# Kernel optimization log

Hardware: AMD Instinct MI355X
Metric: run time of the kernel (lower is better)

Reference implementation:

```python
import jax, jax.numpy as jnp
import numpy as np

T, B, I, H, O = 4096, 16, 64, 256, 1

def setup_inputs() -> dict:
    key = jax.random.key(0)
    ks = jax.random.split(key, 7)
    s_ih = 1.0 / np.sqrt(H)
    return {
        "x": jax.random.normal(ks[0], (T, B, I), dtype=jnp.float32),
        "W_ih": jax.random.normal(ks[1], (4 * H, I), dtype=jnp.float32) * s_ih,
        "W_hh": jax.random.normal(ks[2], (4 * H, H), dtype=jnp.float32) * s_ih,
        "b_ih": jax.random.normal(ks[3], (4 * H,), dtype=jnp.float32) * s_ih,
        "b_hh": jax.random.normal(ks[4], (4 * H,), dtype=jnp.float32) * s_ih,
        "W_lin": jax.random.normal(ks[5], (O, H), dtype=jnp.float32) * s_ih,
        "b_lin": jax.random.normal(ks[6], (O,), dtype=jnp.float32) * s_ih,
        "h0": jnp.zeros((B, H), dtype=jnp.float32),
        "c0": jnp.zeros((B, H), dtype=jnp.float32),
    }

def reference(x, W_ih, W_hh, b_ih, b_hh, W_lin, b_lin, h0, c0):
    # Precompute input contribution for all timesteps: (T, B, 4H)
    x_gates = jnp.einsum('tbi,gi->tbg', x, W_ih) + b_ih + b_hh

    def step(carry, xg):
        h, c = carry
        gates = xg + h @ W_hh.T                      # (B, 4H)
        i, f, g, o = jnp.split(gates, 4, axis=-1)    # PyTorch gate order i|f|g|o
        i = jax.nn.sigmoid(i)
        f = jax.nn.sigmoid(f)
        g = jnp.tanh(g)
        o = jax.nn.sigmoid(o)
        c = f * c + i * g
        h = o * jnp.tanh(c)
        return (h, c), None

    (hT, cT), _ = jax.lax.scan(step, (h0, c0), x_gates)
    # encoder_out[-1] == hT for single-layer unidirectional LSTM; dropout p=0 is identity
    y = jax.nn.sigmoid(hT @ W_lin.T + b_lin)         # (B, O)
    return y
```

## Files before the change

kernel.cpp:

```cpp
#include <hip/hip_runtime.h>
#include <hip/hip_bf16.h>


typedef _Float16 f16x2 __attribute__((ext_vector_type(2)));
typedef _Float16 f16x4 __attribute__((ext_vector_type(4)));
typedef int      i32x4 __attribute__((ext_vector_type(4)));

#define T_STEPS 4096
#define BATCH   16
#define IN      64
#define HID     256
#define G4      1024

__device__ __forceinline__ float fdot2(f16x2 a, f16x2 b, float c) {
#if __has_builtin(__builtin_amdgcn_fdot2)
    return __builtin_amdgcn_fdot2(a, b, c, false);
#else
    return c + (float)a.x * (float)b.x + (float)a.y * (float)b.y;
#endif
}

__device__ __forceinline__ float fast_rcp(float x) {
#if __has_builtin(__builtin_amdgcn_rcpf)
    return __builtin_amdgcn_rcpf(x);
#else
    return 1.0f / x;
#endif
}

__device__ __forceinline__ float sigf(float x) {
    return fast_rcp(1.0f + __expf(-x));
}
__device__ __forceinline__ float tanh_fast(float x) {
    return 2.0f * sigf(2.0f * x) - 1.0f;
}

__global__ __launch_bounds__(256) void xg_precompute(
    const float* __restrict__ x, const float* __restrict__ W_ih,
    const float* __restrict__ b_ih, const float* __restrict__ b_hh,
    _Float16* __restrict__ xg)
{
    const int b   = blockIdx.x;
    const int t0  = blockIdx.y * 128;
    const int tid = threadIdx.x;

    __shared__ __align__(16) f16x2 xs2[IN / 2];

    f16x2 wih[4][32];
    float bias[4];
    const float2* W2 = (const float2*)W_ih;
    #pragma unroll
    for (int g = 0; g < 4; ++g) {
        const int r = tid + g * 256;
        #pragma unroll
        for (int m = 0; m < 32; ++m) {
            float2 v = W2[r * 32 + m];
            wih[g][m] = f16x2{(_Float16)v.x, (_Float16)v.y};
        }
        bias[g] = b_ih[r] + b_hh[r];
    }

    for (int tt = 0; tt < 128; ++tt) {
        const int t = t0 + tt;
        if (tid < 32) {
            float2 v = ((const float2*)x)[(t * BATCH + b) * 32 + tid];
            xs2[tid] = f16x2{(_Float16)v.x, (_Float16)v.y};
        }
        __syncthreads();
        float acc[4] = {bias[0], bias[1], bias[2], bias[3]};
        #pragma unroll
        for (int m = 0; m < 32; ++m) {
            f16x2 xv = xs2[m];
            #pragma unroll
            for (int g = 0; g < 4; ++g) acc[g] = fdot2(wih[g][m], xv, acc[g]);
        }
        f16x4 v4 = f16x4{(_Float16)acc[0], (_Float16)acc[1],
                         (_Float16)acc[2], (_Float16)acc[3]};
        ((f16x4*)xg)[(t * BATCH + b) * 256 + tid] = v4;
        __syncthreads();
    }
}

__global__ __launch_bounds__(1024, 4) void lstm_mfma(
    const float* __restrict__ W_hh,  const float* __restrict__ W_lin,
    const float* __restrict__ b_lin, const float* __restrict__ h0,
    const float* __restrict__ c0,    const _Float16* __restrict__ xg,
    float* __restrict__ out)
{
    const int b   = blockIdx.x;
    const int tid = threadIdx.x;
    const int w   = tid >> 6;
    const int l   = tid & 63;
    const int col = l & 15;
    const int g4  = l >> 4;

    __shared__ __align__(16) signed char hs[2][256];
    __shared__ float esh[256];

    const int u = w * 16 + col;

    const float4* Wh4 = (const float4*)W_hh;
    float qs[4], ksc[4];
    {
        float rm[4];
        #pragma unroll
        for (int g = 0; g < 4; ++g) {
            const int row = g * 256 + u;
            float m = 0.0f;
            #pragma unroll
            for (int c = 0; c < 4; ++c) {
                #pragma unroll
                for (int d = 0; d < 4; ++d) {
                    float4 v = Wh4[row * 64 + 16 * c + 4 * g4 + d];
                    m = fmaxf(m, fmaxf(fmaxf(fabsf(v.x), fabsf(v.y)),
                                       fmaxf(fabsf(v.z), fabsf(v.w))));
                }
            }
            rm[g] = m;
        }
        #pragma unroll
        for (int g = 0; g < 4; ++g) {
            rm[g] = fmaxf(rm[g], __shfl_xor(rm[g], 16, 64));
            rm[g] = fmaxf(rm[g], __shfl_xor(rm[g], 32, 64));
            rm[g] = fmaxf(rm[g], 1e-20f);
            qs[g]  = 127.0f / rm[g];
            ksc[g] = rm[g] * (1.0f / 16129.0f);
        }
    }
    i32x4 wf[4][4];
    #pragma unroll
    for (int g = 0; g < 4; ++g) {
        const int row = g * 256 + u;
        #pragma unroll
        for (int c = 0; c < 4; ++c) {
            union { int i[4]; i32x4 v; } uu;
            #pragma unroll
            for (int d = 0; d < 4; ++d) {
                float4 v = Wh4[row * 64 + 16 * c + 4 * g4 + d];
                int b0 = (int)rintf(v.x * qs[g]) & 255;
                int b1 = (int)rintf(v.y * qs[g]) & 255;
                int b2 = (int)rintf(v.z * qs[g]) & 255;
                int b3 = (int)rintf(v.w * qs[g]) & 255;
                uu.i[d] = b0 | (b1 << 8) | (b2 << 16) | (b3 << 24);
            }
            wf[g][c] = uu.v;
        }
    }

    const float MAGIC = 12582912.0f;
    float cst  = c0[b * HID + u];
    float hval = h0[b * HID + u];
    if (l < 16) {
        union { float f; int i; } m0;
        m0.f = __builtin_fmaf(hval, 127.0f, MAGIC);
        hs[0][u] = (signed char)(m0.i & 0xff);
    }

    union XU { uint2 i; f16x4 h; };
    const uint2* xp = (const uint2*)xg + b * 256 + u;
    XU xc; xc.i = *xp;
    xp += BATCH * 256;

    for (int t = 0; t < T_STEPS; ++t) {
        __syncthreads();

        const uint4* hsv = (const uint4*)(&hs[t & 1][0]);
        union AU { uint4 q; i32x4 v; } a0, a1, a2, a3;
        a0.q = hsv[g4];
        a1.q = hsv[4 + g4];
        a2.q = hsv[8 + g4];
        a3.q = hsv[12 + g4];

        XU xn;
        if (t + 1 < T_STEPS) { xn.i = *xp; xp += BATCH * 256; }
        else                 { xn = xc; }

        i32x4 acc0 = {0, 0, 0, 0};
        i32x4 acc1 = {0, 0, 0, 0};
        i32x4 acc2 = {0, 0, 0, 0};
        i32x4 acc3 = {0, 0, 0, 0};

        acc0 = __builtin_amdgcn_mfma_i32_16x16x64_i8(a0.v, wf[0][0], acc0, 0, 0, 0);
        acc1 = __builtin_amdgcn_mfma_i32_16x16x64_i8(a0.v, wf[1][0], acc1, 0, 0, 0);
        acc2 = __builtin_amdgcn_mfma_i32_16x16x64_i8(a0.v, wf[2][0], acc2, 0, 0, 0);
        acc3 = __builtin_amdgcn_mfma_i32_16x16x64_i8(a0.v, wf[3][0], acc3, 0, 0, 0);
        acc0 = __builtin_amdgcn_mfma_i32_16x16x64_i8(a1.v, wf[0][1], acc0, 0, 0, 0);
        acc1 = __builtin_amdgcn_mfma_i32_16x16x64_i8(a1.v, wf[1][1], acc1, 0, 0, 0);
        acc2 = __builtin_amdgcn_mfma_i32_16x16x64_i8(a1.v, wf[2][1], acc2, 0, 0, 0);
        acc3 = __builtin_amdgcn_mfma_i32_16x16x64_i8(a1.v, wf[3][1], acc3, 0, 0, 0);
        acc0 = __builtin_amdgcn_mfma_i32_16x16x64_i8(a2.v, wf[0][2], acc0, 0, 0, 0);
        acc1 = __builtin_amdgcn_mfma_i32_16x16x64_i8(a2.v, wf[1][2], acc1, 0, 0, 0);
        acc2 = __builtin_amdgcn_mfma_i32_16x16x64_i8(a2.v, wf[2][2], acc2, 0, 0, 0);
        acc3 = __builtin_amdgcn_mfma_i32_16x16x64_i8(a2.v, wf[3][2], acc3, 0, 0, 0);
        acc0 = __builtin_amdgcn_mfma_i32_16x16x64_i8(a3.v, wf[0][3], acc0, 0, 0, 0);
        acc1 = __builtin_amdgcn_mfma_i32_16x16x64_i8(a3.v, wf[1][3], acc1, 0, 0, 0);
        acc2 = __builtin_amdgcn_mfma_i32_16x16x64_i8(a3.v, wf[2][3], acc2, 0, 0, 0);
        acc3 = __builtin_amdgcn_mfma_i32_16x16x64_i8(a3.v, wf[3][3], acc3, 0, 0, 0);

        float gi = sigf((float)acc0[0] * ksc[0] + (float)xc.h[0]);
        float gf = sigf((float)acc1[0] * ksc[1] + (float)xc.h[1]);
        float gg = tanh_fast((float)acc2[0] * ksc[2] + (float)xc.h[2]);
        float go = sigf((float)acc3[0] * ksc[3] + (float)xc.h[3]);
        cst  = gf * cst + gi * gg;
        hval = go * tanh_fast(cst);
        if (l < 16) {
            union { float f; int i; } mg;
            mg.f = __builtin_fmaf(hval, 127.0f, MAGIC);
            hs[(t + 1) & 1][u] = (signed char)(mg.i & 0xff);
        }
        xc = xn;
    }

    if (l < 16) esh[u] = hval * W_lin[u];
    __syncthreads();
    if (tid == 0) {
        float z = b_lin[0];
        for (int n = 0; n < 256; ++n) z += esh[n];
        out[b] = sigf(z);
    }
}

#define NTHR 768
#define KC   11
#define REGC 8
#define LDSC 3
#define HPAD 264
#define WT_OFF   0
#define HB_OFF   147456
#define PS_OFF   148512
#define ESH_OFF  156704
#define SMEM_BYTES 157728
typedef _Float16 f16x8 __attribute__((ext_vector_type(8)));

__global__ __launch_bounds__(NTHR, 3) void lstm_fb(
    const float* __restrict__ x,     const float* __restrict__ W_ih,
    const float* __restrict__ W_hh,  const float* __restrict__ b_ih,
    const float* __restrict__ b_hh,  const float* __restrict__ W_lin,
    const float* __restrict__ b_lin, const float* __restrict__ h0,
    const float* __restrict__ c0,    float* __restrict__ out)
{
    const int b   = blockIdx.x;
    const int tid = threadIdx.x;
    const int j   = tid & 255;
    const int s   = tid >> 8;

    extern __shared__ __align__(16) char smem[];
    f16x8*    wt8  = (f16x8*)(smem + WT_OFF);
    _Float16* hbuf = (_Float16*)(smem + HB_OFF);
    float4*   psum = (float4*)(smem + PS_OFF);
    float*    esh  = (float*)(smem + ESH_OFF);

    f16x2 wr[128];
    const float4* Wh4 = (const float4*)W_hh;
    #pragma unroll
    for (int g = 0; g < 4; ++g) {
        const int r = j + 256 * g;
        #pragma unroll
        for (int c = 0; c < REGC; ++c) {
            const int f4i = r * 64 + (88 * s + 8 * c) / 4;
            float4 a = Wh4[f4i];
            float4 d = Wh4[f4i + 1];
            wr[g * 32 + c * 4 + 0] = f16x2{(_Float16)a.x, (_Float16)a.y};
            wr[g * 32 + c * 4 + 1] = f16x2{(_Float16)a.z, (_Float16)a.w};
            wr[g * 32 + c * 4 + 2] = f16x2{(_Float16)d.x, (_Float16)d.y};
            wr[g * 32 + c * 4 + 3] = f16x2{(_Float16)d.z, (_Float16)d.w};
        }
        #pragma unroll
        for (int c = 0; c < LDSC; ++c) {
            const int k0 = 88 * s + 8 * (REGC + c);
            union { f16x8 v; f16x2 p[4]; } u;
            if (k0 < 256) {
                float4 a = Wh4[r * 64 + k0 / 4];
                float4 d = Wh4[r * 64 + k0 / 4 + 1];
                u.p[0] = f16x2{(_Float16)a.x, (_Float16)a.y};
                u.p[1] = f16x2{(_Float16)a.z, (_Float16)a.w};
                u.p[2] = f16x2{(_Float16)d.x, (_Float16)d.y};
                u.p[3] = f16x2{(_Float16)d.z, (_Float16)d.w};
            } else {
                u.p[0] = f16x2{0, 0}; u.p[1] = f16x2{0, 0};
                u.p[2] = f16x2{0, 0}; u.p[3] = f16x2{0, 0};
            }
            wt8[(g * LDSC + c) * NTHR + tid] = u.v;
        }
    }

    float bias[4] = {0.f, 0.f, 0.f, 0.f};
    if (s == 0) {
        #pragma unroll
        for (int g = 0; g < 4; ++g)
            bias[g] = b_ih[j + g * 256] + b_hh[j + g * 256];
    }

    float cst = 0.f, hval = 0.f;
    if (s == 0) {
        cst  = c0[b * HID + j];
        hval = h0[b * HID + j];
        hbuf[j] = (_Float16)hval;
    }
    if (tid < 8) {
        hbuf[256 + tid]        = (_Float16)0.f;
        hbuf[HPAD + 256 + tid] = (_Float16)0.f;
    }

    for (int t = 0; t < T_STEPS; ++t) {
        __syncthreads();
        const f16x8* hb = (const f16x8*)(hbuf + (t & 1) * HPAD);

        float acc[4] = {0.f, 0.f, 0.f, 0.f};
        if (s != 0) {
            const float4* Wi4 = (const float4*)W_ih;
            const float4* xv4 = (const float4*)(x + ((size_t)t * BATCH + b) * IN)
                                + (s - 1) * 8;
            #pragma unroll
            for (int q = 0; q < 8; ++q) {
                float4 xv = xv4[q];
                #pragma unroll
                for (int g = 0; g < 4; ++g) {
                    float4 wv = Wi4[(j + 256 * g) * 16 + (s - 1) * 8 + q];
                    acc[g] += wv.x * xv.x + wv.y * xv.y + wv.z * xv.z + wv.w * xv.w;
                }
            }
        }
        #pragma unroll
        for (int c = 0; c < REGC; ++c) {
            union { f16x8 v; f16x2 p[4]; } hu;
            hu.v = hb[s * KC + c];
            #pragma unroll
            for (int uu = 0; uu < 4; ++uu) {
                #pragma unroll
                for (int g = 0; g < 4; ++g)
                    acc[g] = fdot2(wr[g * 32 + c * 4 + uu], hu.p[uu], acc[g]);
            }
        }
        #pragma unroll
        for (int c = 0; c < LDSC; ++c) {
            union { f16x8 v; f16x2 p[4]; } hu;
            hu.v = hb[s * KC + REGC + c];
            #pragma unroll
            for (int g = 0; g < 4; ++g) {
                union { f16x8 v; f16x2 p[4]; } wu;
                wu.v = wt8[(g * LDSC + c) * NTHR + tid];
                #pragma unroll
                for (int uu = 0; uu < 4; ++uu)
                    acc[g] = fdot2(wu.p[uu], hu.p[uu], acc[g]);
            }
        }
        if (s != 0)
            psum[(s - 1) * 256 + j] = float4{acc[0], acc[1], acc[2], acc[3]};
        __syncthreads();
        if (s == 0) {
            float4 p1 = psum[j];
            float4 p2 = psum[256 + j];
            float gi = sigf(acc[0] + p1.x + p2.x + bias[0]);
            float gf = sigf(acc[1] + p1.y + p2.y + bias[1]);
            float gg = tanh_fast(acc[2] + p1.z + p2.z + bias[2]);
            float go = sigf(acc[3] + p1.w + p2.w + bias[3]);
            cst  = gf * cst + gi * gg;
            hval = go * tanh_fast(cst);
            hbuf[((t + 1) & 1) * HPAD + j] = (_Float16)hval;
        }
    }

    if (s == 0) esh[j] = hval * W_lin[j];
    __syncthreads();
    if (tid == 0) {
        float z = b_lin[0];
        for (int n = 0; n < 256; ++n) z += esh[n];
        out[b] = sigf(z);
    }
}

extern "C" void kernel_launch(void* const* d_in, const int* in_sizes, int n_in,
                              void* d_out, int out_size, void* d_ws, size_t ws_size,
                              hipStream_t stream) {
    const float* x     = (const float*)d_in[0];
    const float* W_ih  = (const float*)d_in[1];
    const float* W_hh  = (const float*)d_in[2];
    const float* b_ih  = (const float*)d_in[3];
    const float* b_hh  = (const float*)d_in[4];
    const float* W_lin = (const float*)d_in[5];
    const float* b_lin = (const float*)d_in[6];
    const float* h0    = (const float*)d_in[7];
    const float* c0    = (const float*)d_in[8];
    float* out = (float*)d_out;

    const size_t need = (size_t)T_STEPS * BATCH * G4 * sizeof(_Float16);
    if (ws_size >= need) {
        _Float16* xg = (_Float16*)d_ws;
        xg_precompute<<<dim3(BATCH, 32), 256, 0, stream>>>(x, W_ih, b_ih, b_hh, xg);
        lstm_mfma<<<dim3(BATCH), 1024, 0, stream>>>(
            W_hh, W_lin, b_lin, h0, c0, xg, out);
    } else {
        (void)hipFuncSetAttribute((const void*)lstm_fb,
                                  hipFuncAttributeMaxDynamicSharedMemorySize,
                                  SMEM_BYTES);
        lstm_fb<<<dim3(BATCH), NTHR, SMEM_BYTES, stream>>>(
            x, W_ih, W_hh, b_ih, b_hh, W_lin, b_lin, h0, c0, out);
    }
}
```

Baseline: 3.163 ms.

## Split recurrent matvec between MFMA and per-lane sdot4 on idle lanes

Halves the MFMA work per step by keeping only the first two K-chunks of W_hh on the matrix cores. The second half of the hidden dimension is computed with scalar int8 dot4 instructions, where each lane handles one gate row from register-resident weights. The partial sums are then gathered back to the owning lanes with ds_bpermute. The aim is to shorten the serial MFMA dependency chain per timestep, at the cost of extra LDS reads, 32 more weight registers and cross-lane permutes.

```diff
diff --git a/kernel.cpp b/kernel.cpp
--- a/kernel.cpp
+++ b/kernel.cpp
@@ -17,6 +17,18 @@
     return __builtin_amdgcn_fdot2(a, b, c, false);
 #else
     return c + (float)a.x * (float)b.x + (float)a.y * (float)b.y;
+#endif
+}
+
+__device__ __forceinline__ int sdot4(int a, int b, int c) {
+#if __has_builtin(__builtin_amdgcn_sdot4)
+    return __builtin_amdgcn_sdot4(a, b, c, false);
+#else
+    c += (int)(signed char)(a & 0xff)         * (int)(signed char)(b & 0xff);
+    c += (int)(signed char)((a >> 8) & 0xff)  * (int)(signed char)((b >> 8) & 0xff);
+    c += (int)(signed char)((a >> 16) & 0xff) * (int)(signed char)((b >> 16) & 0xff);
+    c += (int)(signed char)(a >> 24)          * (int)(signed char)(b >> 24);
+    return c;
 #endif
 }
 
@@ -127,12 +139,13 @@
             ksc[g] = rm[g] * (1.0f / 16129.0f);
         }
     }
-    i32x4 wf[4][4];
+
+    i32x4 wf[4][2];
     #pragma unroll
     for (int g = 0; g < 4; ++g) {
         const int row = g * 256 + u;
         #pragma unroll
-        for (int c = 0; c < 4; ++c) {
+        for (int c = 0; c < 2; ++c) {
             union { int i[4]; i32x4 v; } uu;
             #pragma unroll
             for (int d = 0; d < 4; ++d) {
@@ -147,6 +160,27 @@
         }
     }
 
+    const float qsd = (g4 & 2) ? ((g4 & 1) ? qs[3] : qs[2])
+                               : ((g4 & 1) ? qs[1] : qs[0]);
+    int wd[32];
+    {
+        const int rg = g4 * 256 + u;
+        #pragma unroll
+        for (int q = 0; q < 32; ++q) {
+            float4 v = Wh4[rg * 64 + 32 + q];
+            int b0 = (int)rintf(v.x * qsd) & 255;
+            int b1 = (int)rintf(v.y * qsd) & 255;
+            int b2 = (int)rintf(v.z * qsd) & 255;
+            int b3 = (int)rintf(v.w * qsd) & 255;
+            wd[q] = b0 | (b1 << 8) | (b2 << 16) | (b3 << 24);
+        }
+    }
+
+    const int bp0 = (col)      << 2;
+    const int bp1 = (16 + col) << 2;
+    const int bp2 = (32 + col) << 2;
+    const int bp3 = (48 + col) << 2;
+
     const float MAGIC = 12582912.0f;
     float cst  = c0[b * HID + u];
     float hval = h0[b * HID + u];
@@ -165,11 +199,10 @@
         __syncthreads();
 
         const uint4* hsv = (const uint4*)(&hs[t & 1][0]);
-        union AU { uint4 q; i32x4 v; } a0, a1, a2, a3;
+
+        union AU { uint4 q; i32x4 v; } a0, a1;
         a0.q = hsv[g4];
         a1.q = hsv[4 + g4];
-        a2.q = hsv[8 + g4];
-        a3.q = hsv[12 + g4];
 
         XU xn;
         if (t + 1 < T_STEPS) { xn.i = *xp; xp += BATCH * 256; }
@@ -188,19 +221,42 @@
         acc1 = __builtin_amdgcn_mfma_i32_16x16x64_i8(a1.v, wf[1][1], acc1, 0, 0, 0);
         acc2 = __builtin_amdgcn_mfma_i32_16x16x64_i8(a1.v, wf[2][1], acc2, 0, 0, 0);
         acc3 = __builtin_amdgcn_mfma_i32_16x16x64_i8(a1.v, wf[3][1], acc3, 0, 0, 0);
-        acc0 = __builtin_amdgcn_mfma_i32_16x16x64_i8(a2.v, wf[0][2], acc0, 0, 0, 0);
-        acc1 = __builtin_amdgcn_mfma_i32_16x16x64_i8(a2.v, wf[1][2], acc1, 0, 0, 0);
-        acc2 = __builtin_amdgcn_mfma_i32_16x16x64_i8(a2.v, wf[2][2], acc2, 0, 0, 0);
-        acc3 = __builtin_amdgcn_mfma_i32_16x16x64_i8(a2.v, wf[3][2], acc3, 0, 0, 0);
-        acc0 = __builtin_amdgcn_mfma_i32_16x16x64_i8(a3.v, wf[0][3], acc0, 0, 0, 0);
-        acc1 = __builtin_amdgcn_mfma_i32_16x16x64_i8(a3.v, wf[1][3], acc1, 0, 0, 0);
-        acc2 = __builtin_amdgcn_mfma_i32_16x16x64_i8(a3.v, wf[2][3], acc2, 0, 0, 0);
-        acc3 = __builtin_amdgcn_mfma_i32_16x16x64_i8(a3.v, wf[3][3], acc3, 0, 0, 0);
-
-        float gi = sigf((float)acc0[0] * ksc[0] + (float)xc.h[0]);
-        float gf = sigf((float)acc1[0] * ksc[1] + (float)xc.h[1]);
-        float gg = tanh_fast((float)acc2[0] * ksc[2] + (float)xc.h[2]);
-        float go = sigf((float)acc3[0] * ksc[3] + (float)xc.h[3]);
+
+        int da0 = 0, da1 = 0, da2 = 0, da3 = 0;
+        #pragma unroll
+        for (int qb = 0; qb < 2; ++qb) {
+            uint4 q0 = hsv[8 + qb * 4 + 0];
+            uint4 q1 = hsv[8 + qb * 4 + 1];
+            uint4 q2 = hsv[8 + qb * 4 + 2];
+            uint4 q3 = hsv[8 + qb * 4 + 3];
+            da0 = sdot4((int)q0.x, wd[qb * 16 + 0],  da0);
+            da1 = sdot4((int)q0.y, wd[qb * 16 + 1],  da1);
+            da2 = sdot4((int)q0.z, wd[qb * 16 + 2],  da2);
+            da3 = sdot4((int)q0.w, wd[qb * 16 + 3],  da3);
+            da0 = sdot4((int)q1.x, wd[qb * 16 + 4],  da0);
+            da1 = sdot4((int)q1.y, wd[qb * 16 + 5],  da1);
+            da2 = sdot4((int)q1.z, wd[qb * 16 + 6],  da2);
+            da3 = sdot4((int)q1.w, wd[qb * 16 + 7],  da3);
+            da0 = sdot4((int)q2.x, wd[qb * 16 + 8],  da0);
+            da1 = sdot4((int)q2.y, wd[qb * 16 + 9],  da1);
+            da2 = sdot4((int)q2.z, wd[qb * 16 + 10], da2);
+            da3 = sdot4((int)q2.w, wd[qb * 16 + 11], da3);
+            da0 = sdot4((int)q3.x, wd[qb * 16 + 12], da0);
+            da1 = sdot4((int)q3.y, wd[qb * 16 + 13], da1);
+            da2 = sdot4((int)q3.z, wd[qb * 16 + 14], da2);
+            da3 = sdot4((int)q3.w, wd[qb * 16 + 15], da3);
+        }
+        const int dacc = (da0 + da1) + (da2 + da3);
+
+        const int dp0 = __builtin_amdgcn_ds_bpermute(bp0, dacc);
+        const int dp1 = __builtin_amdgcn_ds_bpermute(bp1, dacc);
+        const int dp2 = __builtin_amdgcn_ds_bpermute(bp2, dacc);
+        const int dp3 = __builtin_amdgcn_ds_bpermute(bp3, dacc);
+
+        float gi = sigf((float)(acc0[0] + dp0) * ksc[0] + (float)xc.h[0]);
+        float gf = sigf((float)(acc1[0] + dp1) * ksc[1] + (float)xc.h[1]);
+        float gg = tanh_fast((float)(acc2[0] + dp2) * ksc[2] + (float)xc.h[2]);
+        float go = sigf((float)(acc3[0] + dp3) * ksc[3] + (float)xc.h[3]);
         cst  = gf * cst + gi * gg;
         hval = go * tanh_fast(cst);
         if (l < 16) {
```

Result: slower. 4.850 ms (+53.3%).

## Offload last K-chunk of recurrent matmul from MFMA to per-lane sdot4

Applied to the files above, without the earlier changes.

Drops the fourth group of four int8 MFMAs per step. That last 64-wide slice of the hidden dimension is now computed with per-lane sdot4 dot products on broadcast h values, and the partial sums are redistributed across lane groups with swizzle and shuffle. The aim is to shorten the serial MFMA dependency chain on the per-timestep critical path by running VALU work alongside the matrix core. In exchange it adds 16 readlanes, 16 sdot4 operations and several cross-lane shuffles per step, plus extra registers for the weight slice.

```diff
diff --git a/kernel.cpp b/kernel.cpp
--- a/kernel.cpp
+++ b/kernel.cpp
@@ -17,6 +17,26 @@
     return __builtin_amdgcn_fdot2(a, b, c, false);
 #else
     return c + (float)a.x * (float)b.x + (float)a.y * (float)b.y;
+#endif
+}
+
+__device__ __forceinline__ int sdot4(int a, int b, int c) {
+#if __has_builtin(__builtin_amdgcn_sdot4)
+    return __builtin_amdgcn_sdot4(a, b, c, false);
+#else
+    c += (int)(signed char)(a & 0xff)         * (int)(signed char)(b & 0xff);
+    c += (int)(signed char)((a >> 8) & 0xff)  * (int)(signed char)((b >> 8) & 0xff);
+    c += (int)(signed char)((a >> 16) & 0xff) * (int)(signed char)((b >> 16) & 0xff);
+    c += (int)(signed char)(a >> 24)          * (int)(signed char)(b >> 24);
+    return c;
+#endif
+}
+
+__device__ __forceinline__ int xor16_lane(int x) {
+#if __has_builtin(__builtin_amdgcn_ds_swizzle)
+    return __builtin_amdgcn_ds_swizzle(x, 0x401F);
+#else
+    return __shfl_xor(x, 16, 64);
 #endif
 }
 
@@ -127,12 +147,13 @@
             ksc[g] = rm[g] * (1.0f / 16129.0f);
         }
     }
-    i32x4 wf[4][4];
+
+    i32x4 wf[4][3];
     #pragma unroll
     for (int g = 0; g < 4; ++g) {
         const int row = g * 256 + u;
         #pragma unroll
-        for (int c = 0; c < 4; ++c) {
+        for (int c = 0; c < 3; ++c) {
             union { int i[4]; i32x4 v; } uu;
             #pragma unroll
             for (int d = 0; d < 4; ++d) {
@@ -147,6 +168,22 @@
         }
     }
 
+    const float qsd = (g4 & 2) ? ((g4 & 1) ? qs[3] : qs[2])
+                               : ((g4 & 1) ? qs[1] : qs[0]);
+    int wd[16];
+    {
+        const int rg = g4 * 256 + u;
+        #pragma unroll
+        for (int q = 0; q < 16; ++q) {
+            float4 v = Wh4[rg * 64 + 48 + q];
+            int b0 = (int)rintf(v.x * qsd) & 255;
+            int b1 = (int)rintf(v.y * qsd) & 255;
+            int b2 = (int)rintf(v.z * qsd) & 255;
+            int b3 = (int)rintf(v.w * qsd) & 255;
+            wd[q] = b0 | (b1 << 8) | (b2 << 16) | (b3 << 24);
+        }
+    }
+
     const float MAGIC = 12582912.0f;
     float cst  = c0[b * HID + u];
     float hval = h0[b * HID + u];
@@ -165,7 +202,8 @@
         __syncthreads();
 
         const uint4* hsv = (const uint4*)(&hs[t & 1][0]);
-        union AU { uint4 q; i32x4 v; } a0, a1, a2, a3;
+
+        union AU { uint4 q; int i[4]; i32x4 v; } a0, a1, a2, a3;
         a0.q = hsv[g4];
         a1.q = hsv[4 + g4];
         a2.q = hsv[8 + g4];
@@ -174,6 +212,11 @@
         XU xn;
         if (t + 1 < T_STEPS) { xn.i = *xp; xp += BATCH * 256; }
         else                 { xn = xc; }
+
+        int hu[16];
+        #pragma unroll
+        for (int j = 0; j < 16; ++j)
+            hu[j] = __builtin_amdgcn_readlane(a3.i[j & 3], 16 * (j >> 2));
 
         i32x4 acc0 = {0, 0, 0, 0};
         i32x4 acc1 = {0, 0, 0, 0};
@@ -192,15 +235,33 @@
         acc1 = __builtin_amdgcn_mfma_i32_16x16x64_i8(a2.v, wf[1][2], acc1, 0, 0, 0);
         acc2 = __builtin_amdgcn_mfma_i32_16x16x64_i8(a2.v, wf[2][2], acc2, 0, 0, 0);
         acc3 = __builtin_amdgcn_mfma_i32_16x16x64_i8(a2.v, wf[3][2], acc3, 0, 0, 0);
-        acc0 = __builtin_amdgcn_mfma_i32_16x16x64_i8(a3.v, wf[0][3], acc0, 0, 0, 0);
-        acc1 = __builtin_amdgcn_mfma_i32_16x16x64_i8(a3.v, wf[1][3], acc1, 0, 0, 0);
-        acc2 = __builtin_amdgcn_mfma_i32_16x16x64_i8(a3.v, wf[2][3], acc2, 0, 0, 0);
-        acc3 = __builtin_amdgcn_mfma_i32_16x16x64_i8(a3.v, wf[3][3], acc3, 0, 0, 0);
-
-        float gi = sigf((float)acc0[0] * ksc[0] + (float)xc.h[0]);
-        float gf = sigf((float)acc1[0] * ksc[1] + (float)xc.h[1]);
-        float gg = tanh_fast((float)acc2[0] * ksc[2] + (float)xc.h[2]);
-        float go = sigf((float)acc3[0] * ksc[3] + (float)xc.h[3]);
+
+        int d0 = 0, d1 = 0, d2 = 0, d3 = 0;
+        #pragma unroll
+        for (int j = 0; j < 4; ++j) {
+            d0 = sdot4(hu[4 * j + 0], wd[4 * j + 0], d0);
+            d1 = sdot4(hu[4 * j + 1], wd[4 * j + 1], d1);
+            d2 = sdot4(hu[4 * j + 2], wd[4 * j + 2], d2);
+            d3 = sdot4(hu[4 * j + 3], wd[4 * j + 3], d3);
+        }
+        const int dacc = (d0 + d1) + (d2 + d3);
+
+        const int n16 = xor16_lane(dacc);
+        const int n32 = __shfl_xor(dacc, 32, 64);
+        const int n48 = __shfl_xor(n16, 32, 64);
+        const bool s0 = (g4 & 1) != 0;
+        const bool s1 = (g4 & 2) != 0;
+        const int pa0 = s0 ? n16 : dacc, pa1 = s0 ? dacc : n16;
+        const int pc0 = s0 ? n48 : n32,  pc1 = s0 ? n32 : n48;
+        const int dp0 = s1 ? pc0 : pa0;
+        const int dp1 = s1 ? pc1 : pa1;
+        const int dp2 = s1 ? pa0 : pc0;
+        const int dp3 = s1 ? pa1 : pc1;
+
+        float gi = sigf((float)(acc0[0] + dp0) * ksc[0] + (float)xc.h[0]);
+        float gf = sigf((float)(acc1[0] + dp1) * ksc[1] + (float)xc.h[1]);
+        float gg = tanh_fast((float)(acc2[0] + dp2) * ksc[2] + (float)xc.h[2]);
+        float go = sigf((float)(acc3[0] + dp3) * ksc[3] + (float)xc.h[3]);
         cst  = gf * cst + gi * gg;
         hval = go * tanh_fast(cst);
         if (l < 16) {
```

After: 4.813 ms. +52.2%, slower.
